# Kernel tuning notes

Measured on AMD Instinct MI355X. Metric: run time of the kernel, lower is better.

Reference implementation:

```python
import jax, jax.numpy as jnp
import numpy as np

N_NODES = 50000
N_EDGES = 800000
F_NODE = 64
F_EDGE = 32
F_GLOBAL = 32
OUT_DIM = 64
N_GRAPHS = 256


def setup_inputs() -> dict:
    key = jax.random.key(0)
    ks = jax.random.split(key, 8)
    x = jax.random.normal(ks[0], (N_NODES, F_NODE), dtype=jnp.float32)
    edge_index = jax.random.randint(ks[1], (2, N_EDGES), 0, N_NODES, dtype=jnp.int64)
    edge_attr = jax.random.normal(ks[2], (N_EDGES, F_EDGE), dtype=jnp.float32)
    u = jax.random.normal(ks[3], (N_GRAPHS, F_GLOBAL), dtype=jnp.float32)
    batch = jnp.sort(jax.random.randint(ks[4], (N_NODES,), 0, N_GRAPHS, dtype=jnp.int64))
    # params (scaled like default Linear init)
    W1 = jax.random.normal(ks[5], (F_NODE + F_EDGE, OUT_DIM), dtype=jnp.float32) / np.sqrt(F_NODE + F_EDGE)
    b1 = jnp.zeros((OUT_DIM,), dtype=jnp.float32)
    W2 = jax.random.normal(ks[6], (F_NODE + OUT_DIM + F_GLOBAL, OUT_DIM), dtype=jnp.float32) / np.sqrt(F_NODE + OUT_DIM + F_GLOBAL)
    b2 = jnp.zeros((OUT_DIM,), dtype=jnp.float32)
    return {"x": x, "edge_index": edge_index, "edge_attr": edge_attr,
            "u": u, "batch": batch, "W1": W1, "b1": b1, "W2": W2, "b2": b2}


def reference(x, edge_index, edge_attr, u, batch, W1, b1, W2, b2):
    dest, src = edge_index[0], edge_index[1]
    # gather source node features + edge attrs -> [E, F_NODE + F_EDGE]
    edge_info = jnp.concatenate([x[src], edge_attr], axis=1)
    # node_mlp_1: Linear + ReLU
    edge_messages = jax.nn.relu(edge_info @ W1 + b1)  # [E, OUT_DIM]
    # scatter-sum into destination nodes
    aggregated = jax.ops.segment_sum(edge_messages, dest, num_segments=x.shape[0])  # [N, OUT_DIM]
    # concat node, aggregated messages, per-graph global
    node_info = jnp.concatenate([x, aggregated, u[batch]], axis=1)  # [N, F_NODE+OUT_DIM+F_GLOBAL]
    # node_mlp_2: Linear + ReLU
    return jax.nn.relu(node_info @ W2 + b2)  # [N, OUT_DIM]
```

## Files before the change

kernel.cpp:

```cpp
#include <hip/hip_runtime.h>
#include <hip/hip_bf16.h>

typedef __attribute__((ext_vector_type(8))) short short8;
typedef __attribute__((ext_vector_type(4))) float f32x4;

constexpr int NN = 50000;
constexpr int NE = 800000;
constexpr int FN = 64;
constexpr int FE = 32;
constexpr int FG = 32;
constexpr int OD = 64;
constexpr int NG = 256;

constexpr int SCAN_B = 256;
constexpr int NBLK = (NN + SCAN_B - 1) / SCAN_B;

constexpr int SLOTS_CAP = 1350000;
constexpr int NWIN_CAP  = SLOTS_CAP / 16;

constexpr int XCVT_BLOCKS = (NN * FN / 8 + 255) / 256;
constexpr int PRE_BLOCKS  = XCVT_BLOCKS + (NG * 64) / 256;

constexpr int AGG_BLOCKS = 2048;
constexpr int AGG_WAVES  = AGG_BLOCKS * 4;
constexpr int NWIN_N = NN / 16;
constexpr int NODE_BLOCKS = 782;
constexpr int NODE_WAVES  = NODE_BLOCKS * 4;

static __device__ __forceinline__ unsigned pack_bf16(float a, float b) {
    __hip_bfloat162 h = __float22bfloat162_rn(float2{a, b});
    return *reinterpret_cast<unsigned*>(&h);
}

__global__ __launch_bounds__(256) void k_pre(const float* __restrict__ x,
                                             unsigned* __restrict__ xb32,
                                             const float* __restrict__ u,
                                             const float* __restrict__ W2,
                                             const float* __restrict__ b2,
                                             float* __restrict__ uW2b,
                                             int* __restrict__ cnt) {
    if (blockIdx.x >= XCVT_BLOCKS) {
        const int lane = threadIdx.x & 63;
        float wcol[FG];
#pragma unroll
        for (int k = 0; k < FG; ++k) wcol[k] = W2[(FN + OD + k) * OD + lane];
        const float bias = b2[lane];
        int g = ((blockIdx.x - XCVT_BLOCKS) * 256 + threadIdx.x) >> 6;
        g = __builtin_amdgcn_readfirstlane(g);
        if (g >= NG) return;
        const float* __restrict__ urow = u + (size_t)g * FG;
        float acc = bias;
#pragma unroll
        for (int k = 0; k < FG; ++k) acc = fmaf(urow[k], wcol[k], acc);
        uW2b[(size_t)g * OD + lane] = acc;
        return;
    }
    const int i = blockIdx.x * 256 + threadIdx.x;
    if (i < NN) cnt[i] = 0;
    if (i >= NN * FN / 8) return;
    const float4* p = (const float4*)(x + (size_t)i * 8);
    float4 f0 = p[0], f1 = p[1];
    uint4 o;
    o.x = pack_bf16(f0.x, f0.y);
    o.y = pack_bf16(f0.z, f0.w);
    o.z = pack_bf16(f1.x, f1.y);
    o.w = pack_bf16(f1.z, f1.w);
    ((uint4*)xb32)[i] = o;
}

__global__ __launch_bounds__(256) void k_hist(const int* __restrict__ ei,
                                              int* __restrict__ cnt) {
    const int e = blockIdx.x * blockDim.x + threadIdx.x;
    if (e < NE) atomicAdd(&cnt[ei[e]], 1);
}

__global__ __launch_bounds__(SCAN_B) void k_scan1(const int* __restrict__ cnt,
                                                  int* __restrict__ pstart,
                                                  int* __restrict__ bsum) {
    __shared__ int lds[SCAN_B];
    const int i = blockIdx.x * SCAN_B + threadIdx.x;
    const int v = (i < NN) ? (((cnt[i] + 15) >> 4) << 4) : 0;
    lds[threadIdx.x] = v;
    __syncthreads();
#pragma unroll
    for (int off = 1; off < SCAN_B; off <<= 1) {
        int t = (threadIdx.x >= off) ? lds[threadIdx.x - off] : 0;
        __syncthreads();
        lds[threadIdx.x] += t;
        __syncthreads();
    }
    const int incl = lds[threadIdx.x];
    if (i < NN) pstart[i] = incl - v;
    if (threadIdx.x == SCAN_B - 1) bsum[blockIdx.x] = incl;
}

__global__ __launch_bounds__(SCAN_B) void k_scan23(int* __restrict__ pstart,
                                                   const int* __restrict__ bsum,
                                                   const int* __restrict__ cnt,
                                                   int* __restrict__ cursor,
                                                   int* __restrict__ winend) {
    __shared__ int lds[SCAN_B];
    const int t = threadIdx.x;
    lds[t] = (t < NBLK) ? bsum[t] : 0;
    __syncthreads();
#pragma unroll
    for (int off = 1; off < SCAN_B; off <<= 1) {
        int tv = (t >= off) ? lds[t - off] : 0;
        __syncthreads();
        lds[t] += tv;
        __syncthreads();
    }
    const int boff = (blockIdx.x == 0) ? 0 : lds[blockIdx.x - 1];

    const int i = blockIdx.x * SCAN_B + t;
    if (i < NN) {
        const int cn = cnt[i];
        const int pc = ((cn + 15) >> 4) << 4;
        const int s = pstart[i] + boff;
        pstart[i] = s;
        cursor[i] = s;
        const int end = s + cn;
        const int w0 = s >> 4;
        const int w1 = (s + pc) >> 4;
        for (int w = w0; w < w1; ++w) winend[w] = end;
        if (i == NN - 1) pstart[NN] = s + pc;
    }
}

__global__ __launch_bounds__(256) void k_scat2(const int* __restrict__ ei,
                                               const float* __restrict__ ea,
                                               int* __restrict__ cursor,
                                               int* __restrict__ bucket_src,
                                               uint4* __restrict__ bucket_ea) {
    const int t = blockIdx.x * 256 + threadIdx.x;
    const int e = t >> 2;
    const int p = t & 3;
    if (e >= NE) return;

    const int lane = threadIdx.x & 63;
    const int dst = ei[e];
    int pos = 0;
    if (p == 0) pos = atomicAdd(&cursor[dst], 1);
    pos = __shfl(pos, lane & ~3);
    if (p == 0) bucket_src[pos] = ei[NE + e];

    const float4* er = (const float4*)(ea + (size_t)e * FE) + 2 * p;
    const float4 f0 = er[0];
    const float4 f1 = er[1];
    uint4 o;
    o.x = pack_bf16(f0.x, f0.y);
    o.y = pack_bf16(f0.z, f0.w);
    o.z = pack_bf16(f1.x, f1.y);
    o.w = pack_bf16(f1.z, f1.w);
    bucket_ea[(size_t)pos * 4 + p] = o;
}

__global__ __launch_bounds__(256) void k_aggw3(const int* __restrict__ bucket_src,
                                               const uint4* __restrict__ bucket_ea,
                                               const unsigned short* __restrict__ xb,
                                               const float* __restrict__ W1,
                                               const float* __restrict__ b1,
                                               const int* __restrict__ pstart,
                                               const int* __restrict__ winend,
                                               unsigned* __restrict__ partial32) {
    const int l = threadIdx.x & 63;
    const int g = l >> 4;
    const int c = l & 15;

    short8 wf[3][4];
#pragma unroll
    for (int t = 0; t < 3; ++t)
#pragma unroll
        for (int b = 0; b < 4; ++b)
#pragma unroll
            for (int i = 0; i < 8; i += 2) {
                const int k = 32 * t + 8 * g + i;
                const unsigned p = pack_bf16(W1[k * OD + (c + 16 * b)],
                                             W1[(k + 1) * OD + (c + 16 * b)]);
                ((unsigned*)&wf[t][b])[i / 2] = p;
            }
    float bias[4];
#pragma unroll
    for (int b = 0; b < 4; ++b) bias[b] = b1[c + 16 * b];

    const int nwin = pstart[NN] >> 4;

    int wv = (blockIdx.x * blockDim.x + threadIdx.x) >> 6;
    wv = __builtin_amdgcn_readfirstlane(wv);

    for (int w = wv; w < nwin; w += AGG_WAVES) {
        const int end = winend[w];
        int slot = w * 16 + c;
        if (slot >= end) slot = end - 1;

        const uint4 qe = bucket_ea[(size_t)(w * 16 + c < end ? slot : slot) * 4 + g];
        const int src = bucket_src[slot];

        const uint4* xr = (const uint4*)(xb + (size_t)src * FN);
        const uint4 q0 = xr[g];
        const uint4 q1 = xr[4 + g];

        const short8 a0 = *(const short8*)&q0;
        const short8 a1 = *(const short8*)&q1;
        const short8 a2 = *(const short8*)&qe;

        float sv[4];
#pragma unroll
        for (int b = 0; b < 4; ++b) {
            f32x4 acc = {0.f, 0.f, 0.f, 0.f};
            acc = __builtin_amdgcn_mfma_f32_16x16x32_bf16(a0, wf[0][b], acc, 0, 0, 0);
            acc = __builtin_amdgcn_mfma_f32_16x16x32_bf16(a1, wf[1][b], acc, 0, 0, 0);
            acc = __builtin_amdgcn_mfma_f32_16x16x32_bf16(a2, wf[2][b], acc, 0, 0, 0);
            float s = 0.0f;
#pragma unroll
            for (int q = 0; q < 4; ++q) {
                const int row = w * 16 + 4 * g + q;
                const float v = fmaxf(acc[q] + bias[b], 0.0f);
                s += (row < end) ? v : 0.0f;
            }
            s += __shfl_xor(s, 16);
            s += __shfl_xor(s, 32);
            sv[b] = s;
        }
        float v = sv[0];
        v = (g == 1) ? sv[1] : v;
        v = (g == 2) ? sv[2] : v;
        v = (g == 3) ? sv[3] : v;

        const float vn = __shfl_xor(v, 1);
        if ((l & 1) == 0)
            partial32[(size_t)w * 32 + (l >> 1)] = pack_bf16(v, vn);
    }
}

__global__ __launch_bounds__(256) void k_red(const unsigned* __restrict__ partial32,
                                             const int* __restrict__ pstart,
                                             unsigned* __restrict__ aggb32) {
    const int l = threadIdx.x & 63;
    const int q = l & 31;
    int nb = (blockIdx.x * blockDim.x + threadIdx.x) >> 6;
    nb = __builtin_amdgcn_readfirstlane(nb);
    const int n = 2 * nb + (l >> 5);
    if (n >= NN) return;

    const int w0 = pstart[n] >> 4;
    const int w1 = pstart[n + 1] >> 4;
    float c0 = 0.0f, c1 = 0.0f;
    for (int w = w0; w < w1; ++w) {
        const unsigned uu = partial32[(size_t)w * 32 + q];
        c0 += __uint_as_float(uu << 16);
        c1 += __uint_as_float(uu & 0xffff0000u);
    }
    aggb32[(size_t)n * 32 + q] = pack_bf16(c0, c1);
}

__global__ __launch_bounds__(256) void k_nodem(const unsigned short* __restrict__ xb,
                                               const unsigned short* __restrict__ aggb,
                                               const int* __restrict__ bat,
                                               const float* __restrict__ uW2b,
                                               const float* __restrict__ W2,
                                               float* __restrict__ out) {
    const int l = threadIdx.x & 63;
    const int g = l >> 4;
    const int c = l & 15;

    short8 wf[4][4];
#pragma unroll
    for (int t = 0; t < 4; ++t)
#pragma unroll
        for (int b = 0; b < 4; ++b)
#pragma unroll
            for (int i = 0; i < 8; i += 2) {
                const int k = 32 * t + 8 * g + i;
                const unsigned p = pack_bf16(W2[k * OD + (c + 16 * b)],
                                             W2[(k + 1) * OD + (c + 16 * b)]);
                ((unsigned*)&wf[t][b])[i / 2] = p;
            }

    int wv = (blockIdx.x * blockDim.x + threadIdx.x) >> 6;
    wv = __builtin_amdgcn_readfirstlane(wv);

    for (int w = wv; w < NWIN_N; w += NODE_WAVES) {
        const int n0 = w * 16;
        const uint4* xr = (const uint4*)(xb + (size_t)(n0 + c) * FN);
        const uint4* ar = (const uint4*)(aggb + (size_t)(n0 + c) * OD);
        uint4 qx0 = xr[g], qx1 = xr[4 + g];
        uint4 qa0 = ar[g], qa1 = ar[4 + g];
        short8 a0 = *(short8*)&qx0, a1 = *(short8*)&qx1;
        short8 a2 = *(short8*)&qa0, a3 = *(short8*)&qa1;

        int bq[4];
#pragma unroll
        for (int q = 0; q < 4; ++q) bq[q] = bat[n0 + g * 4 + q];

#pragma unroll
        for (int b = 0; b < 4; ++b) {
            f32x4 acc = {0.f, 0.f, 0.f, 0.f};
            acc = __builtin_amdgcn_mfma_f32_16x16x32_bf16(a0, wf[0][b], acc, 0, 0, 0);
            acc = __builtin_amdgcn_mfma_f32_16x16x32_bf16(a1, wf[1][b], acc, 0, 0, 0);
            acc = __builtin_amdgcn_mfma_f32_16x16x32_bf16(a2, wf[2][b], acc, 0, 0, 0);
            acc = __builtin_amdgcn_mfma_f32_16x16x32_bf16(a3, wf[3][b], acc, 0, 0, 0);
#pragma unroll
            for (int q = 0; q < 4; ++q) {
                const int n = n0 + g * 4 + q;
                const float val = acc[q] + uW2b[(size_t)bq[q] * OD + c + 16 * b];
                out[(size_t)n * OD + c + 16 * b] = fmaxf(val, 0.0f);
            }
        }
    }
}

extern "C" void kernel_launch(void* const* d_in, const int* in_sizes, int n_in,
                              void* d_out, int out_size, void* d_ws, size_t ws_size,
                              hipStream_t stream) {
    const float* x    = (const float*)d_in[0];
    const int*   ei   = (const int*)d_in[1];
    const float* ea   = (const float*)d_in[2];
    const float* u    = (const float*)d_in[3];
    const int*   bat  = (const int*)d_in[4];
    const float* W1   = (const float*)d_in[5];
    const float* b1   = (const float*)d_in[6];
    const float* W2   = (const float*)d_in[7];
    const float* b2   = (const float*)d_in[8];
    float* out = (float*)d_out;

    char* ws = (char*)d_ws;
    auto alloc = [&](size_t bytes) {
        char* p = ws;
        ws += (bytes + 255) & ~size_t(255);
        return p;
    };
    unsigned short* xb   = (unsigned short*)alloc((size_t)NN * FN * 2);
    unsigned short* aggb = (unsigned short*)alloc((size_t)NN * OD * 2);
    float* uW2b    = (float*)alloc((size_t)NG * OD * sizeof(float));
    int*   cnt     = (int*)alloc((size_t)NN * sizeof(int));
    int*   pstart  = (int*)alloc((size_t)(NN + 1) * sizeof(int));
    int*   cursor  = (int*)alloc((size_t)NN * sizeof(int));
    int*   bsum    = (int*)alloc((size_t)NBLK * sizeof(int));
    int*   winend  = (int*)alloc((size_t)NWIN_CAP * sizeof(int));
    int*   bucket_src = (int*)alloc((size_t)SLOTS_CAP * sizeof(int));
    uint4* bucket_ea  = (uint4*)alloc((size_t)SLOTS_CAP * 64);
    unsigned* partial = (unsigned*)alloc((size_t)NWIN_CAP * 32 * 4);

    k_pre<<<dim3(PRE_BLOCKS), dim3(256), 0, stream>>>(x, (unsigned*)xb, u, W2, b2, uW2b, cnt);

    k_hist<<<dim3((NE + 255) / 256), dim3(256), 0, stream>>>(ei, cnt);
    k_scan1<<<dim3(NBLK), dim3(SCAN_B), 0, stream>>>(cnt, pstart, bsum);
    k_scan23<<<dim3(NBLK), dim3(SCAN_B), 0, stream>>>(pstart, bsum, cnt, cursor, winend);

    k_scat2<<<dim3((NE * 4 + 255) / 256), dim3(256), 0, stream>>>(ei, ea, cursor, bucket_src, bucket_ea);

    k_aggw3<<<dim3(AGG_BLOCKS), dim3(256), 0, stream>>>(bucket_src, bucket_ea, xb, W1, b1,
                                                        pstart, winend, partial);

    k_red<<<dim3((NN * 32 + 255) / 256), dim3(256), 0, stream>>>(partial, pstart, (unsigned*)aggb);

    k_nodem<<<dim3(NODE_BLOCKS), dim3(256), 0, stream>>>(xb, aggb, bat, uW2b, W2, out);
}
```

Measured before the change: 156.1 us.

## Scatter only (src,edge) indices and stream gathers into LDS with multi-stage prefetch

The scatter kernel now writes only (src, edge id) pairs per bucket slot instead of also converting and copying edge attributes to bf16. The aggregation kernel gathers fp32 edge attributes and bf16 node rows directly into swizzled LDS using global_load_lds with a 4-deep software pipeline, then converts edge features to bf16 in registers before the MFMA. Each wave handles a contiguous chunk of windows. This cuts the write and reread of the bucketed edge-attribute array and tries to hide gather latency, at the cost of 64KB LDS per block, lower occupancy and hand-managed vmcnt waits that need to be correct.

```diff
diff --git a/kernel.cpp b/kernel.cpp
--- a/kernel.cpp
+++ b/kernel.cpp
@@ -15,14 +15,14 @@
 constexpr int SCAN_B = 256;
 constexpr int NBLK = (NN + SCAN_B - 1) / SCAN_B;
 
-constexpr int SLOTS_CAP = 1350000;
-constexpr int NWIN_CAP  = SLOTS_CAP / 16;
+constexpr int SLOTS_MAX = NE + 15 * NN;
+constexpr int NWIN_MAX  = SLOTS_MAX / 16;
 
 constexpr int XCVT_BLOCKS = (NN * FN / 8 + 255) / 256;
 constexpr int PRE_BLOCKS  = XCVT_BLOCKS + (NG * 64) / 256;
 
-constexpr int AGG_BLOCKS = 2048;
-constexpr int AGG_WAVES  = AGG_BLOCKS * 4;
+constexpr int AGG4_BLOCKS = 512;
+constexpr int AGG4_WAVES  = AGG4_BLOCKS * 4;
 constexpr int NWIN_N = NN / 16;
 constexpr int NODE_BLOCKS = 782;
 constexpr int NODE_WAVES  = NODE_BLOCKS * 4;
@@ -30,6 +30,12 @@
 static __device__ __forceinline__ unsigned pack_bf16(float a, float b) {
     __hip_bfloat162 h = __float22bfloat162_rn(float2{a, b});
     return *reinterpret_cast<unsigned*>(&h);
+}
+
+static __device__ __forceinline__ void gl16(const void* gsrc, void* ldst) {
+    __builtin_amdgcn_global_load_lds(
+        (const __attribute__((address_space(1))) void*)gsrc,
+        (__attribute__((address_space(3))) void*)ldst, 16, 0, 0);
 }
 
 __global__ __launch_bounds__(256) void k_pre(const float* __restrict__ x,
@@ -127,42 +133,27 @@
     }
 }
 
-__global__ __launch_bounds__(256) void k_scat2(const int* __restrict__ ei,
-                                               const float* __restrict__ ea,
-                                               int* __restrict__ cursor,
-                                               int* __restrict__ bucket_src,
-                                               uint4* __restrict__ bucket_ea) {
-    const int t = blockIdx.x * 256 + threadIdx.x;
-    const int e = t >> 2;
-    const int p = t & 3;
-    if (e >= NE) return;
-
-    const int lane = threadIdx.x & 63;
-    const int dst = ei[e];
-    int pos = 0;
-    if (p == 0) pos = atomicAdd(&cursor[dst], 1);
-    pos = __shfl(pos, lane & ~3);
-    if (p == 0) bucket_src[pos] = ei[NE + e];
-
-    const float4* er = (const float4*)(ea + (size_t)e * FE) + 2 * p;
-    const float4 f0 = er[0];
-    const float4 f1 = er[1];
-    uint4 o;
-    o.x = pack_bf16(f0.x, f0.y);
-    o.y = pack_bf16(f0.z, f0.w);
-    o.z = pack_bf16(f1.x, f1.y);
-    o.w = pack_bf16(f1.z, f1.w);
-    bucket_ea[(size_t)pos * 4 + p] = o;
-}
-
-__global__ __launch_bounds__(256) void k_aggw3(const int* __restrict__ bucket_src,
-                                               const uint4* __restrict__ bucket_ea,
-                                               const unsigned short* __restrict__ xb,
-                                               const float* __restrict__ W1,
-                                               const float* __restrict__ b1,
-                                               const int* __restrict__ pstart,
-                                               const int* __restrict__ winend,
-                                               unsigned* __restrict__ partial32) {
+__global__ __launch_bounds__(256) void k_scatter(const int* __restrict__ ei,
+                                                 int* __restrict__ cursor,
+                                                 int2* __restrict__ bucket) {
+    const int e = blockIdx.x * blockDim.x + threadIdx.x;
+    if (e < NE) {
+        const int dst = ei[e];
+        const int src = ei[NE + e];
+        const int pos = atomicAdd(&cursor[dst], 1);
+        bucket[pos] = make_int2(src, e);
+    }
+}
+
+__global__ __launch_bounds__(256, 2) void k_aggw4(const int2* __restrict__ bucket,
+                                                  const float* __restrict__ ea,
+                                                  const unsigned short* __restrict__ xb,
+                                                  const float* __restrict__ W1,
+                                                  const float* __restrict__ b1,
+                                                  const int* __restrict__ pstart,
+                                                  const int* __restrict__ winend,
+                                                  unsigned* __restrict__ partial32) {
+    __shared__ char ldsbuf[65536];
     const int l = threadIdx.x & 63;
     const int g = l >> 4;
     const int c = l & 15;
@@ -184,27 +175,88 @@
     for (int b = 0; b < 4; ++b) bias[b] = b1[c + 16 * b];
 
     const int nwin = pstart[NN] >> 4;
-
-    int wv = (blockIdx.x * blockDim.x + threadIdx.x) >> 6;
-    wv = __builtin_amdgcn_readfirstlane(wv);
-
-    for (int w = wv; w < nwin; w += AGG_WAVES) {
-        const int end = winend[w];
-        int slot = w * 16 + c;
-        if (slot >= end) slot = end - 1;
-
-        const uint4 qe = bucket_ea[(size_t)(w * 16 + c < end ? slot : slot) * 4 + g];
-        const int src = bucket_src[slot];
-
-        const uint4* xr = (const uint4*)(xb + (size_t)src * FN);
-        const uint4 q0 = xr[g];
-        const uint4 q1 = xr[4 + g];
-
-        const short8 a0 = *(const short8*)&q0;
-        const short8 a1 = *(const short8*)&q1;
-        const short8 a2 = *(const short8*)&qe;
-
-        float sv[4];
+    int wid = (blockIdx.x * blockDim.x + threadIdx.x) >> 6;
+    wid = __builtin_amdgcn_readfirstlane(wid);
+    const int chunk = (nwin + AGG4_WAVES - 1) / AGG4_WAVES;
+    const int c0 = wid * chunk;
+    int len = nwin - c0;
+    if (len > chunk) len = chunk;
+    if (len <= 0) return;
+
+    char* myl = &ldsbuf[((threadIdx.x >> 6) & 3) * 16384];
+    const int swz = (((l & 7) ^ ((l >> 3) & 7)) << 4);
+
+    auto ldSE = [&](int G) -> int2 {
+        int wr = 4 * G + (l >> 4);
+        if (wr > len - 1) wr = len - 1;
+        return bucket[(size_t)(c0 + wr) * 16 + (l & 15)];
+    };
+    auto ldEND = [&](int G) -> int {
+        int wr = 4 * G + (l & 3);
+        if (wr > len - 1) wr = len - 1;
+        return winend[c0 + wr];
+    };
+
+    auto issue = [&](int2 seH, int qd, int p) {
+        char* dst = myl + p * 4096;
+#pragma unroll
+        for (int half = 0; half < 2; ++half) {
+            const int srcLane = (qd << 4) + (half << 3) + (l >> 3);
+            int sv = __shfl(seH.x, srcLane);
+            int ev = __shfl(seH.y, srcLane);
+            sv = ((unsigned)sv < (unsigned)NN) ? sv : 0;
+            ev = ((unsigned)ev < (unsigned)NE) ? ev : 0;
+            gl16((const char*)ea + ((size_t)ev * 128 + swz), dst + half * 1024);
+            gl16((const char*)xb + ((size_t)sv * 128 + swz), dst + 2048 + half * 1024);
+        }
+    };
+
+    int2 se0 = ldSE(0);
+    int2 seH = ldSE(1), seM = ldSE(2), seP = ldSE(3);
+    int enH = ldEND(0), enM = ldEND(1), enP = ldEND(2);
+#pragma unroll
+    for (int i = 0; i < 4; ++i) {
+        int wr = (i > len - 1) ? (len - 1) : i;
+        issue(se0, wr, i);
+    }
+
+    for (int i = 0; i < len; ++i) {
+        const int p = i & 3;
+        const int w = c0 + i;
+
+        asm volatile("s_waitcnt vmcnt(12)" ::: "memory");
+        __builtin_amdgcn_sched_barrier(0);
+
+        const char* base = myl + p * 4096;
+        const float4 e0 = *(const float4*)(base + c * 128 + (((2 * g) ^ (c & 7)) << 4));
+        const float4 e1 = *(const float4*)(base + c * 128 + (((2 * g + 1) ^ (c & 7)) << 4));
+        const uint4  x0 = *(const uint4*)(base + 2048 + c * 128 + ((g ^ (c & 7)) << 4));
+        const uint4  x1 = *(const uint4*)(base + 2048 + c * 128 + (((g + 4) ^ (c & 7)) << 4));
+        const int end = __shfl(enH, p);
+
+        __builtin_amdgcn_sched_barrier(0);
+        {
+            int wn = i + 4;
+            if (wn > len - 1) wn = len - 1;
+            int qd = wn - 4 * ((i >> 2) + 1);
+            qd = qd < 0 ? 0 : (qd > 3 ? 3 : qd);
+            issue(seH, qd, p);
+        }
+        if (p == 3) {
+            seH = seM; seM = seP; seP = ldSE((i >> 2) + 4);
+            enH = enM; enM = enP; enP = ldEND((i >> 2) + 3);
+        }
+
+        const short8 a0 = *(const short8*)&x0;
+        const short8 a1 = *(const short8*)&x1;
+        uint4 q2;
+        q2.x = pack_bf16(e0.x, e0.y);
+        q2.y = pack_bf16(e0.z, e0.w);
+        q2.z = pack_bf16(e1.x, e1.y);
+        q2.w = pack_bf16(e1.z, e1.w);
+        const short8 a2 = *(const short8*)&q2;
+
+        float sv4[4];
 #pragma unroll
         for (int b = 0; b < 4; ++b) {
             f32x4 acc = {0.f, 0.f, 0.f, 0.f};
@@ -220,17 +272,18 @@
             }
             s += __shfl_xor(s, 16);
             s += __shfl_xor(s, 32);
-            sv[b] = s;
+            sv4[b] = s;
         }
-        float v = sv[0];
-        v = (g == 1) ? sv[1] : v;
-        v = (g == 2) ? sv[2] : v;
-        v = (g == 3) ? sv[3] : v;
+        float v = sv4[0];
+        v = (g == 1) ? sv4[1] : v;
+        v = (g == 2) ? sv4[2] : v;
+        v = (g == 3) ? sv4[3] : v;
 
         const float vn = __shfl_xor(v, 1);
         if ((l & 1) == 0)
             partial32[(size_t)w * 32 + (l >> 1)] = pack_bf16(v, vn);
     }
+    asm volatile("s_waitcnt vmcnt(0)" ::: "memory");
 }
 
 __global__ __launch_bounds__(256) void k_red(const unsigned* __restrict__ partial32,
@@ -337,10 +390,9 @@
     int*   pstart  = (int*)alloc((size_t)(NN + 1) * sizeof(int));
     int*   cursor  = (int*)alloc((size_t)NN * sizeof(int));
     int*   bsum    = (int*)alloc((size_t)NBLK * sizeof(int));
-    int*   winend  = (int*)alloc((size_t)NWIN_CAP * sizeof(int));
-    int*   bucket_src = (int*)alloc((size_t)SLOTS_CAP * sizeof(int));
-    uint4* bucket_ea  = (uint4*)alloc((size_t)SLOTS_CAP * 64);
-    unsigned* partial = (unsigned*)alloc((size_t)NWIN_CAP * 32 * 4);
+    int*   winend  = (int*)alloc((size_t)NWIN_MAX * sizeof(int));
+    int2*  bucket  = (int2*)alloc((size_t)SLOTS_MAX * sizeof(int2));
+    unsigned* partial = (unsigned*)alloc((size_t)NWIN_MAX * 32 * 4);
 
     k_pre<<<dim3(PRE_BLOCKS), dim3(256), 0, stream>>>(x, (unsigned*)xb, u, W2, b2, uW2b, cnt);
 
@@ -348,10 +400,10 @@
     k_scan1<<<dim3(NBLK), dim3(SCAN_B), 0, stream>>>(cnt, pstart, bsum);
     k_scan23<<<dim3(NBLK), dim3(SCAN_B), 0, stream>>>(pstart, bsum, cnt, cursor, winend);
 
-    k_scat2<<<dim3((NE * 4 + 255) / 256), dim3(256), 0, stream>>>(ei, ea, cursor, bucket_src, bucket_ea);
-
-    k_aggw3<<<dim3(AGG_BLOCKS), dim3(256), 0, stream>>>(bucket_src, bucket_ea, xb, W1, b1,
-                                                        pstart, winend, partial);
+    k_scatter<<<dim3((NE + 255) / 256), dim3(256), 0, stream>>>(ei, cursor, bucket);
+
+    k_aggw4<<<dim3(AGG4_BLOCKS), dim3(256), 0, stream>>>(bucket, ea, xb, W1, b1,
+                                                         pstart, winend, partial);
 
     k_red<<<dim3((NN * 32 + 255) / 256), dim3(256), 0, stream>>>(partial, pstart, (unsigned*)aggb);
 
```

New measurement: 172.1 us. 1.1x slower.
